# Performance work log

Hardware: AMD Instinct MI355X
Metric: run time of the kernel (lower is better)

Reference implementation:

```python
import jax, jax.numpy as jnp
import numpy as np

L, D = 32768, 1024  # timesteps, independent book-feature columns


def setup_inputs() -> dict:
    key = jax.random.key(0)
    k1, k2 = jax.random.split(key)
    data = jax.random.normal(k1, (L, D), dtype=jnp.float32)
    first_offset = jax.random.normal(k2, (1, D), dtype=jnp.float32)
    alpha = jnp.float32(0.01)  # EWMA smoothing constant in (0, 1)
    return {"data": data, "first_offset": first_offset, "alpha": alpha}


def reference(data, first_offset, alpha):
    # Exact math of ewma_vectorized_safe (vmapped over columns):
    #   y_t = (1 - alpha) * y_{t-1} + alpha * x_t,  y_{-1} = first_offset
    # The original implements this with a chunked power-scaled cumsum trick
    # for precision; a single linear scan computes the identical recurrence.
    decay = 1.0 - alpha

    def step(carry, x_t):  # carry: (D,), x_t: (D,)
        y_t = decay * carry + alpha * x_t
        return y_t, y_t

    last, out = jax.lax.scan(step, first_offset[0], data)  # out: (L, D)
    return out, last[None, :]  # matches (out, out[-1:]) with out_axes=(1, 1)
```

## Files before the change

### kernel.cpp

```cpp
#include <hip/hip_runtime.h>


#define LT   32768
#define DC   1024
#define TCH  32
#define CCH  (LT / TCH)
#define TPB  256
#define D4   (DC / 4)

typedef float nf4 __attribute__((ext_vector_type(4)));

__global__ void ewma_phase1(const nf4* __restrict__ data4,
                            nf4* __restrict__ zend4,
                            const float* __restrict__ alpha_p) {
    const float alpha = alpha_p[0];
    const float decay = 1.0f - alpha;
    const int tid = threadIdx.x;
    const int c = blockIdx.x;
    const nf4* p = data4 + (size_t)c * TCH * D4 + tid;
    float z0 = 0.f, z1 = 0.f, z2 = 0.f, z3 = 0.f;
#pragma unroll 8
    for (int i = 0; i < TCH; ++i) {
        nf4 x = p[(size_t)i * D4];
        z0 = fmaf(decay, z0, alpha * x.x);
        z1 = fmaf(decay, z1, alpha * x.y);
        z2 = fmaf(decay, z2, alpha * x.z);
        z3 = fmaf(decay, z3, alpha * x.w);
    }
    nf4 zv; zv.x = z0; zv.y = z1; zv.z = z2; zv.w = z3;
    zend4[c * D4 + tid] = zv;
}

__global__ void ewma_phase2(const float* __restrict__ zend,
                            const float* __restrict__ first,
                            float* __restrict__ carry,
                            const float* __restrict__ alpha_p) {
    const float alpha = alpha_p[0];
    const float decay = 1.0f - alpha;
    float r = decay;
    r *= r; r *= r; r *= r; r *= r; r *= r;

    const int lane = threadIdx.x & 63;
    const int d = (blockIdx.x * blockDim.x + threadIdx.x) >> 6;
    constexpr int CPL = CCH / 64;

    float e[CPL];
#pragma unroll
    for (int j = 0; j < CPL; ++j)
        e[j] = zend[(lane * CPL + j) * DC + d];

    float A = 0.f;
#pragma unroll
    for (int j = 0; j < CPL; ++j) A = fmaf(r, A, e[j]);

    float q = r;
    q *= q; q *= q; q *= q; q *= q;

    float y = A;
    float p = q;
#pragma unroll
    for (int o = 1; o < 64; o <<= 1) {
        float prev = __shfl_up(y, o, 64);
        if (lane >= o) y = fmaf(p, prev, y);
        p = p * p;
    }
    float excl = __shfl_up(y, 1, 64);
    if (lane == 0) excl = 0.f;

    float qpow = 1.f;
    {
        float base = q;
        int e2 = lane;
        while (e2) { if (e2 & 1) qpow *= base; base *= base; e2 >>= 1; }
    }
    float S = fmaf(qpow, first[d], excl);

#pragma unroll
    for (int j = 0; j < CPL; ++j) {
        const int c = lane * CPL + j;
        carry[c * DC + d] = S;
        S = fmaf(r, S, e[j]);
    }
}

__global__ void ewma_phase3(const nf4* __restrict__ data4,
                            const nf4* __restrict__ carry4,
                            nf4* __restrict__ out4,
                            nf4* __restrict__ out_last4,
                            const float* __restrict__ alpha_p) {
    const float alpha = alpha_p[0];
    const float decay = 1.0f - alpha;
    const int tid = threadIdx.x;
    const int c = blockIdx.x;
    const nf4 cin = carry4[c * D4 + tid];
    const nf4* p = data4 + (size_t)c * TCH * D4 + tid;
    nf4* o = out4 + (size_t)c * TCH * D4 + tid;
    float z0 = 0.f, z1 = 0.f, z2 = 0.f, z3 = 0.f, pw = 1.f;
#pragma unroll 8
    for (int i = 0; i < TCH; ++i) {
        nf4 x = p[(size_t)i * D4];
        z0 = fmaf(decay, z0, alpha * x.x);
        z1 = fmaf(decay, z1, alpha * x.y);
        z2 = fmaf(decay, z2, alpha * x.z);
        z3 = fmaf(decay, z3, alpha * x.w);
        pw *= decay;
        nf4 yv;
        yv.x = fmaf(pw, cin.x, z0);
        yv.y = fmaf(pw, cin.y, z1);
        yv.z = fmaf(pw, cin.z, z2);
        yv.w = fmaf(pw, cin.w, z3);
        __builtin_nontemporal_store(yv, &o[(size_t)i * D4]);
    }
    if (c == CCH - 1) {
        nf4 yl;
        yl.x = fmaf(pw, cin.x, z0);
        yl.y = fmaf(pw, cin.y, z1);
        yl.z = fmaf(pw, cin.z, z2);
        yl.w = fmaf(pw, cin.w, z3);
        out_last4[tid] = yl;
    }
}

extern "C" void kernel_launch(void* const* d_in, const int* in_sizes, int n_in,
                              void* d_out, int out_size, void* d_ws, size_t ws_size,
                              hipStream_t stream) {
    const float* data    = (const float*)d_in[0];
    const float* first   = (const float*)d_in[1];
    const float* alpha_p = (const float*)d_in[2];
    float* out = (float*)d_out;

    float* zend  = (float*)d_ws;
    float* carry = zend + (size_t)CCH * DC;

    ewma_phase1<<<CCH, TPB, 0, stream>>>(
        (const nf4*)data, (nf4*)zend, alpha_p);

    ewma_phase2<<<DC / (TPB / 64), TPB, 0, stream>>>(
        zend, first, carry, alpha_p);

    ewma_phase3<<<CCH, TPB, 0, stream>>>(
        (const nf4*)data, (const nf4*)carry, (nf4*)out,
        (nf4*)(out + (size_t)LT * DC), alpha_p);
}
```

Baseline: 84.50 us.

## Write local scan to output in phase 1 and fix up in place in phase 3

Phase 1 now writes the chunk-local partial scan straight to the output buffer. Phase 3 then reads that buffer back, adds the decayed carry, and writes the result in place instead of re-reading the input and recomputing the scan. Input loads in phase 1 become nontemporal, and phase 3's stores become ordinary cached stores. The aim is better cache behaviour, since the output written in phase 1 may still be resident in the large last-level cache when phase 3 runs. The cost is an extra full-size write pass, so total traffic becomes read+write, then read+write, instead of read, then read+write.

```diff
diff --git a/kernel.cpp b/kernel.cpp
--- a/kernel.cpp
+++ b/kernel.cpp
@@ -10,31 +10,35 @@
 
 typedef float nf4 __attribute__((ext_vector_type(4)));
 
-__global__ void ewma_phase1(const nf4* __restrict__ data4,
-                            nf4* __restrict__ zend4,
-                            const float* __restrict__ alpha_p) {
+__global__ void ewma_k1(const nf4* __restrict__ data4,
+                        nf4* __restrict__ out4,
+                        nf4* __restrict__ zend4,
+                        const float* __restrict__ alpha_p) {
     const float alpha = alpha_p[0];
     const float decay = 1.0f - alpha;
     const int tid = threadIdx.x;
     const int c = blockIdx.x;
     const nf4* p = data4 + (size_t)c * TCH * D4 + tid;
+    nf4* o = out4 + (size_t)c * TCH * D4 + tid;
     float z0 = 0.f, z1 = 0.f, z2 = 0.f, z3 = 0.f;
 #pragma unroll 8
     for (int i = 0; i < TCH; ++i) {
-        nf4 x = p[(size_t)i * D4];
+        nf4 x = __builtin_nontemporal_load(&p[(size_t)i * D4]);
         z0 = fmaf(decay, z0, alpha * x.x);
         z1 = fmaf(decay, z1, alpha * x.y);
         z2 = fmaf(decay, z2, alpha * x.z);
         z3 = fmaf(decay, z3, alpha * x.w);
+        nf4 zv; zv.x = z0; zv.y = z1; zv.z = z2; zv.w = z3;
+        o[(size_t)i * D4] = zv;
     }
-    nf4 zv; zv.x = z0; zv.y = z1; zv.z = z2; zv.w = z3;
-    zend4[c * D4 + tid] = zv;
+    nf4 ze; ze.x = z0; ze.y = z1; ze.z = z2; ze.w = z3;
+    zend4[c * D4 + tid] = ze;
 }
 
-__global__ void ewma_phase2(const float* __restrict__ zend,
-                            const float* __restrict__ first,
-                            float* __restrict__ carry,
-                            const float* __restrict__ alpha_p) {
+__global__ void ewma_k2(const float* __restrict__ zend,
+                        const float* __restrict__ first,
+                        float* __restrict__ carry,
+                        const float* __restrict__ alpha_p) {
     const float alpha = alpha_p[0];
     const float decay = 1.0f - alpha;
     float r = decay;
@@ -83,42 +87,30 @@
     }
 }
 
-__global__ void ewma_phase3(const nf4* __restrict__ data4,
-                            const nf4* __restrict__ carry4,
-                            nf4* __restrict__ out4,
-                            nf4* __restrict__ out_last4,
-                            const float* __restrict__ alpha_p) {
+__global__ void ewma_k3(nf4* __restrict__ out4,
+                        const nf4* __restrict__ carry4,
+                        nf4* __restrict__ out_last4,
+                        const float* __restrict__ alpha_p) {
     const float alpha = alpha_p[0];
     const float decay = 1.0f - alpha;
     const int tid = threadIdx.x;
     const int c = blockIdx.x;
     const nf4 cin = carry4[c * D4 + tid];
-    const nf4* p = data4 + (size_t)c * TCH * D4 + tid;
     nf4* o = out4 + (size_t)c * TCH * D4 + tid;
-    float z0 = 0.f, z1 = 0.f, z2 = 0.f, z3 = 0.f, pw = 1.f;
+    float pw = 1.f;
+    nf4 yv;
 #pragma unroll 8
     for (int i = 0; i < TCH; ++i) {
-        nf4 x = p[(size_t)i * D4];
-        z0 = fmaf(decay, z0, alpha * x.x);
-        z1 = fmaf(decay, z1, alpha * x.y);
-        z2 = fmaf(decay, z2, alpha * x.z);
-        z3 = fmaf(decay, z3, alpha * x.w);
+        nf4 v = o[(size_t)i * D4];
         pw *= decay;
-        nf4 yv;
-        yv.x = fmaf(pw, cin.x, z0);
-        yv.y = fmaf(pw, cin.y, z1);
-        yv.z = fmaf(pw, cin.z, z2);
-        yv.w = fmaf(pw, cin.w, z3);
-        __builtin_nontemporal_store(yv, &o[(size_t)i * D4]);
+        yv.x = fmaf(pw, cin.x, v.x);
+        yv.y = fmaf(pw, cin.y, v.y);
+        yv.z = fmaf(pw, cin.z, v.z);
+        yv.w = fmaf(pw, cin.w, v.w);
+        o[(size_t)i * D4] = yv;
     }
-    if (c == CCH - 1) {
-        nf4 yl;
-        yl.x = fmaf(pw, cin.x, z0);
-        yl.y = fmaf(pw, cin.y, z1);
-        yl.z = fmaf(pw, cin.z, z2);
-        yl.w = fmaf(pw, cin.w, z3);
-        out_last4[tid] = yl;
-    }
+    if (c == CCH - 1)
+        out_last4[tid] = yv;
 }
 
 extern "C" void kernel_launch(void* const* d_in, const int* in_sizes, int n_in,
@@ -132,13 +124,13 @@
     float* zend  = (float*)d_ws;
     float* carry = zend + (size_t)CCH * DC;
 
-    ewma_phase1<<<CCH, TPB, 0, stream>>>(
-        (const nf4*)data, (nf4*)zend, alpha_p);
+    ewma_k1<<<CCH, TPB, 0, stream>>>(
+        (const nf4*)data, (nf4*)out, (nf4*)zend, alpha_p);
 
-    ewma_phase2<<<DC / (TPB / 64), TPB, 0, stream>>>(
+    ewma_k2<<<DC / (TPB / 64), TPB, 0, stream>>>(
         zend, first, carry, alpha_p);
 
-    ewma_phase3<<<CCH, TPB, 0, stream>>>(
-        (const nf4*)data, (const nf4*)carry, (nf4*)out,
+    ewma_k3<<<CCH, TPB, 0, stream>>>(
+        (nf4*)out, (const nf4*)carry,
         (nf4*)(out + (size_t)LT * DC), alpha_p);
 }
```

Result: slower. 106.7 us (+26.2%).

## Split columns into two slabs so phase-3 data reads hit cache

Applied to the files above, without the earlier changes.

Runs the three-phase scan as two sequential passes over column halves, each pass launching phase 1, 2 and 3 on a 64 MB data slab with 128-thread blocks. The intent is for phase 3 to re-read data still resident in the large last-level cache after phase 1, rather than fetching it again from HBM. Loops are also fully unrolled, and output stores become regular stores instead of nontemporal ones. The cost is twice as many kernel launches, smaller blocks, and normal stores that may evict cached input.

```diff
diff --git a/kernel.cpp b/kernel.cpp
--- a/kernel.cpp
+++ b/kernel.cpp
@@ -3,23 +3,25 @@
 
 #define LT   32768
 #define DC   1024
+#define NS   2
+#define SW   (DC / NS)
+#define SW4  (SW / 4)
 #define TCH  32
 #define CCH  (LT / TCH)
-#define TPB  256
 #define D4   (DC / 4)
 
 typedef float nf4 __attribute__((ext_vector_type(4)));
 
-__global__ void ewma_phase1(const nf4* __restrict__ data4,
-                            nf4* __restrict__ zend4,
-                            const float* __restrict__ alpha_p) {
+__global__ void ewma_p1(const nf4* __restrict__ data4,
+                        nf4* __restrict__ zend4,
+                        const float* __restrict__ alpha_p, int s) {
     const float alpha = alpha_p[0];
     const float decay = 1.0f - alpha;
-    const int tid = threadIdx.x;
+    const int g = threadIdx.x;
     const int c = blockIdx.x;
-    const nf4* p = data4 + (size_t)c * TCH * D4 + tid;
+    const nf4* p = data4 + (size_t)c * TCH * D4 + s * SW4 + g;
     float z0 = 0.f, z1 = 0.f, z2 = 0.f, z3 = 0.f;
-#pragma unroll 8
+#pragma unroll
     for (int i = 0; i < TCH; ++i) {
         nf4 x = p[(size_t)i * D4];
         z0 = fmaf(decay, z0, alpha * x.x);
@@ -28,26 +30,26 @@
         z3 = fmaf(decay, z3, alpha * x.w);
     }
     nf4 zv; zv.x = z0; zv.y = z1; zv.z = z2; zv.w = z3;
-    zend4[c * D4 + tid] = zv;
+    zend4[(size_t)c * D4 + s * SW4 + g] = zv;
 }
 
-__global__ void ewma_phase2(const float* __restrict__ zend,
-                            const float* __restrict__ first,
-                            float* __restrict__ carry,
-                            const float* __restrict__ alpha_p) {
+__global__ void ewma_p2(const float* __restrict__ zend,
+                        const float* __restrict__ first,
+                        float* __restrict__ carry,
+                        const float* __restrict__ alpha_p, int s) {
     const float alpha = alpha_p[0];
     const float decay = 1.0f - alpha;
     float r = decay;
     r *= r; r *= r; r *= r; r *= r; r *= r;
 
     const int lane = threadIdx.x & 63;
-    const int d = (blockIdx.x * blockDim.x + threadIdx.x) >> 6;
+    const int d = s * SW + ((blockIdx.x * blockDim.x + threadIdx.x) >> 6);
     constexpr int CPL = CCH / 64;
 
     float e[CPL];
 #pragma unroll
     for (int j = 0; j < CPL; ++j)
-        e[j] = zend[(lane * CPL + j) * DC + d];
+        e[j] = zend[(size_t)(lane * CPL + j) * DC + d];
 
     float A = 0.f;
 #pragma unroll
@@ -78,25 +80,25 @@
 #pragma unroll
     for (int j = 0; j < CPL; ++j) {
         const int c = lane * CPL + j;
-        carry[c * DC + d] = S;
+        carry[(size_t)c * DC + d] = S;
         S = fmaf(r, S, e[j]);
     }
 }
 
-__global__ void ewma_phase3(const nf4* __restrict__ data4,
-                            const nf4* __restrict__ carry4,
-                            nf4* __restrict__ out4,
-                            nf4* __restrict__ out_last4,
-                            const float* __restrict__ alpha_p) {
+__global__ void ewma_p3(const nf4* __restrict__ data4,
+                        const nf4* __restrict__ carry4,
+                        nf4* __restrict__ out4,
+                        nf4* __restrict__ out_last4,
+                        const float* __restrict__ alpha_p, int s) {
     const float alpha = alpha_p[0];
     const float decay = 1.0f - alpha;
-    const int tid = threadIdx.x;
+    const int g = threadIdx.x;
     const int c = blockIdx.x;
-    const nf4 cin = carry4[c * D4 + tid];
-    const nf4* p = data4 + (size_t)c * TCH * D4 + tid;
-    nf4* o = out4 + (size_t)c * TCH * D4 + tid;
+    const nf4 cin = carry4[(size_t)c * D4 + s * SW4 + g];
+    const nf4* p = data4 + (size_t)c * TCH * D4 + s * SW4 + g;
+    nf4* o = out4 + (size_t)c * TCH * D4 + s * SW4 + g;
     float z0 = 0.f, z1 = 0.f, z2 = 0.f, z3 = 0.f, pw = 1.f;
-#pragma unroll 8
+#pragma unroll
     for (int i = 0; i < TCH; ++i) {
         nf4 x = p[(size_t)i * D4];
         z0 = fmaf(decay, z0, alpha * x.x);
@@ -109,7 +111,7 @@
         yv.y = fmaf(pw, cin.y, z1);
         yv.z = fmaf(pw, cin.z, z2);
         yv.w = fmaf(pw, cin.w, z3);
-        __builtin_nontemporal_store(yv, &o[(size_t)i * D4]);
+        o[(size_t)i * D4] = yv;
     }
     if (c == CCH - 1) {
         nf4 yl;
@@ -117,7 +119,7 @@
         yl.y = fmaf(pw, cin.y, z1);
         yl.z = fmaf(pw, cin.z, z2);
         yl.w = fmaf(pw, cin.w, z3);
-        out_last4[tid] = yl;
+        out_last4[s * SW4 + g] = yl;
     }
 }
 
@@ -132,13 +134,15 @@
     float* zend  = (float*)d_ws;
     float* carry = zend + (size_t)CCH * DC;
 
-    ewma_phase1<<<CCH, TPB, 0, stream>>>(
-        (const nf4*)data, (nf4*)zend, alpha_p);
+    for (int s = 0; s < NS; ++s) {
+        ewma_p1<<<CCH, SW4, 0, stream>>>(
+            (const nf4*)data, (nf4*)zend, alpha_p, s);
 
-    ewma_phase2<<<DC / (TPB / 64), TPB, 0, stream>>>(
-        zend, first, carry, alpha_p);
+        ewma_p2<<<SW / 4, 256, 0, stream>>>(
+            zend, first, carry, alpha_p, s);
 
-    ewma_phase3<<<CCH, TPB, 0, stream>>>(
-        (const nf4*)data, (const nf4*)carry, (nf4*)out,
-        (nf4*)(out + (size_t)LT * DC), alpha_p);
+        ewma_p3<<<CCH, SW4, 0, stream>>>(
+            (const nf4*)data, (const nf4*)carry, (nf4*)out,
+            (nf4*)(out + (size_t)LT * DC), alpha_p, s);
+    }
 }
```

Result: slower. 100.2 us (+18.6%).

## Fuse three EWMA phases into one cooperative kernel with grid syncs

Applied to the files above, without the earlier changes.

Merges the chunk-reduce, carry-scan, and apply phases into a single cooperative launch separated by grid-wide barriers, and doubles the time chunk length so the whole grid fits co-resident. This removes the inter-kernel launch gaps and halves the intermediate carry buffers. It trades occupancy and grid-sync cost for this, and also replaces nontemporal output stores with regular stores.

```diff
diff --git a/kernel.cpp b/kernel.cpp
--- a/kernel.cpp
+++ b/kernel.cpp
@@ -1,123 +1,126 @@
 #include <hip/hip_runtime.h>
+#include <hip/hip_cooperative_groups.h>
+
+namespace cg = cooperative_groups;
 
 
 #define LT   32768
 #define DC   1024
-#define TCH  32
+#define TCH  64
 #define CCH  (LT / TCH)
 #define TPB  256
 #define D4   (DC / 4)
 
 typedef float nf4 __attribute__((ext_vector_type(4)));
 
-__global__ void ewma_phase1(const nf4* __restrict__ data4,
-                            nf4* __restrict__ zend4,
-                            const float* __restrict__ alpha_p) {
+__global__ __launch_bounds__(TPB, 2)
+void ewma_fused(const nf4* __restrict__ data4,
+                const float* __restrict__ first,
+                const float* __restrict__ alpha_p,
+                nf4* __restrict__ out4,
+                nf4* __restrict__ zend4,
+                float* __restrict__ carry) {
+    cg::grid_group grid = cg::this_grid();
     const float alpha = alpha_p[0];
     const float decay = 1.0f - alpha;
     const int tid = threadIdx.x;
     const int c = blockIdx.x;
-    const nf4* p = data4 + (size_t)c * TCH * D4 + tid;
-    float z0 = 0.f, z1 = 0.f, z2 = 0.f, z3 = 0.f;
+
+    {
+        const nf4* p = data4 + (size_t)c * TCH * D4 + tid;
+        float z0 = 0.f, z1 = 0.f, z2 = 0.f, z3 = 0.f;
 #pragma unroll 8
-    for (int i = 0; i < TCH; ++i) {
-        nf4 x = p[(size_t)i * D4];
-        z0 = fmaf(decay, z0, alpha * x.x);
-        z1 = fmaf(decay, z1, alpha * x.y);
-        z2 = fmaf(decay, z2, alpha * x.z);
-        z3 = fmaf(decay, z3, alpha * x.w);
+        for (int i = 0; i < TCH; ++i) {
+            nf4 x = p[(size_t)i * D4];
+            z0 = fmaf(decay, z0, alpha * x.x);
+            z1 = fmaf(decay, z1, alpha * x.y);
+            z2 = fmaf(decay, z2, alpha * x.z);
+            z3 = fmaf(decay, z3, alpha * x.w);
+        }
+        nf4 zv; zv.x = z0; zv.y = z1; zv.z = z2; zv.w = z3;
+        zend4[(size_t)c * D4 + tid] = zv;
     }
-    nf4 zv; zv.x = z0; zv.y = z1; zv.z = z2; zv.w = z3;
-    zend4[c * D4 + tid] = zv;
-}
 
-__global__ void ewma_phase2(const float* __restrict__ zend,
-                            const float* __restrict__ first,
-                            float* __restrict__ carry,
-                            const float* __restrict__ alpha_p) {
-    const float alpha = alpha_p[0];
-    const float decay = 1.0f - alpha;
-    float r = decay;
-    r *= r; r *= r; r *= r; r *= r; r *= r;
+    grid.sync();
 
-    const int lane = threadIdx.x & 63;
-    const int d = (blockIdx.x * blockDim.x + threadIdx.x) >> 6;
-    constexpr int CPL = CCH / 64;
+    if (c < DC / 4) {
+        const int lane = tid & 63;
+        const int w = tid >> 6;
+        const int d = c * 4 + w;
+        float r = decay;
+        r *= r; r *= r; r *= r; r *= r; r *= r; r *= r;
+        constexpr int CPL = CCH / 64;
 
-    float e[CPL];
+        const float* zend = (const float*)zend4;
+        float e[CPL];
 #pragma unroll
-    for (int j = 0; j < CPL; ++j)
-        e[j] = zend[(lane * CPL + j) * DC + d];
+        for (int j = 0; j < CPL; ++j)
+            e[j] = zend[(size_t)(lane * CPL + j) * DC + d];
 
-    float A = 0.f;
+        float A = 0.f;
 #pragma unroll
-    for (int j = 0; j < CPL; ++j) A = fmaf(r, A, e[j]);
+        for (int j = 0; j < CPL; ++j) A = fmaf(r, A, e[j]);
 
-    float q = r;
-    q *= q; q *= q; q *= q; q *= q;
+        float q = r;
+        q *= q; q *= q; q *= q;
 
-    float y = A;
-    float p = q;
+        float y = A;
+        float pq = q;
 #pragma unroll
-    for (int o = 1; o < 64; o <<= 1) {
-        float prev = __shfl_up(y, o, 64);
-        if (lane >= o) y = fmaf(p, prev, y);
-        p = p * p;
-    }
-    float excl = __shfl_up(y, 1, 64);
-    if (lane == 0) excl = 0.f;
+        for (int o = 1; o < 64; o <<= 1) {
+            float prev = __shfl_up(y, o, 64);
+            if (lane >= o) y = fmaf(pq, prev, y);
+            pq = pq * pq;
+        }
+        float excl = __shfl_up(y, 1, 64);
+        if (lane == 0) excl = 0.f;
 
-    float qpow = 1.f;
-    {
-        float base = q;
-        int e2 = lane;
-        while (e2) { if (e2 & 1) qpow *= base; base *= base; e2 >>= 1; }
-    }
-    float S = fmaf(qpow, first[d], excl);
+        float qpow = 1.f;
+        {
+            float base = q;
+            int e2 = lane;
+            while (e2) { if (e2 & 1) qpow *= base; base *= base; e2 >>= 1; }
+        }
+        float S = fmaf(qpow, first[d], excl);
 
 #pragma unroll
-    for (int j = 0; j < CPL; ++j) {
-        const int c = lane * CPL + j;
-        carry[c * DC + d] = S;
-        S = fmaf(r, S, e[j]);
+        for (int j = 0; j < CPL; ++j) {
+            const int cc = lane * CPL + j;
+            carry[(size_t)cc * DC + d] = S;
+            S = fmaf(r, S, e[j]);
+        }
     }
-}
 
-__global__ void ewma_phase3(const nf4* __restrict__ data4,
-                            const nf4* __restrict__ carry4,
-                            nf4* __restrict__ out4,
-                            nf4* __restrict__ out_last4,
-                            const float* __restrict__ alpha_p) {
-    const float alpha = alpha_p[0];
-    const float decay = 1.0f - alpha;
-    const int tid = threadIdx.x;
-    const int c = blockIdx.x;
-    const nf4 cin = carry4[c * D4 + tid];
-    const nf4* p = data4 + (size_t)c * TCH * D4 + tid;
-    nf4* o = out4 + (size_t)c * TCH * D4 + tid;
-    float z0 = 0.f, z1 = 0.f, z2 = 0.f, z3 = 0.f, pw = 1.f;
+    grid.sync();
+
+    {
+        const nf4 cin = ((const nf4*)carry)[(size_t)c * D4 + tid];
+        const nf4* p = data4 + (size_t)c * TCH * D4 + tid;
+        nf4* o = out4 + (size_t)c * TCH * D4 + tid;
+        float z0 = 0.f, z1 = 0.f, z2 = 0.f, z3 = 0.f, pw = 1.f;
 #pragma unroll 8
-    for (int i = 0; i < TCH; ++i) {
-        nf4 x = p[(size_t)i * D4];
-        z0 = fmaf(decay, z0, alpha * x.x);
-        z1 = fmaf(decay, z1, alpha * x.y);
-        z2 = fmaf(decay, z2, alpha * x.z);
-        z3 = fmaf(decay, z3, alpha * x.w);
-        pw *= decay;
-        nf4 yv;
-        yv.x = fmaf(pw, cin.x, z0);
-        yv.y = fmaf(pw, cin.y, z1);
-        yv.z = fmaf(pw, cin.z, z2);
-        yv.w = fmaf(pw, cin.w, z3);
-        __builtin_nontemporal_store(yv, &o[(size_t)i * D4]);
-    }
-    if (c == CCH - 1) {
-        nf4 yl;
-        yl.x = fmaf(pw, cin.x, z0);
-        yl.y = fmaf(pw, cin.y, z1);
-        yl.z = fmaf(pw, cin.z, z2);
-        yl.w = fmaf(pw, cin.w, z3);
-        out_last4[tid] = yl;
+        for (int i = 0; i < TCH; ++i) {
+            nf4 x = p[(size_t)i * D4];
+            z0 = fmaf(decay, z0, alpha * x.x);
+            z1 = fmaf(decay, z1, alpha * x.y);
+            z2 = fmaf(decay, z2, alpha * x.z);
+            z3 = fmaf(decay, z3, alpha * x.w);
+            pw *= decay;
+            nf4 yv;
+            yv.x = fmaf(pw, cin.x, z0);
+            yv.y = fmaf(pw, cin.y, z1);
+            yv.z = fmaf(pw, cin.z, z2);
+            yv.w = fmaf(pw, cin.w, z3);
+            o[(size_t)i * D4] = yv;
+        }
+        if (c == CCH - 1) {
+            nf4 yl;
+            yl.x = fmaf(pw, cin.x, z0);
+            yl.y = fmaf(pw, cin.y, z1);
+            yl.z = fmaf(pw, cin.z, z2);
+            yl.w = fmaf(pw, cin.w, z3);
+            ((nf4*)(((float*)out4) + (size_t)LT * DC))[tid] = yl;
+        }
     }
 }
 
@@ -132,13 +135,12 @@
     float* zend  = (float*)d_ws;
     float* carry = zend + (size_t)CCH * DC;
 
-    ewma_phase1<<<CCH, TPB, 0, stream>>>(
-        (const nf4*)data, (nf4*)zend, alpha_p);
+    const nf4* data4 = (const nf4*)data;
+    nf4* out4 = (nf4*)out;
+    nf4* zend4 = (nf4*)zend;
 
-    ewma_phase2<<<DC / (TPB / 64), TPB, 0, stream>>>(
-        zend, first, carry, alpha_p);
-
-    ewma_phase3<<<CCH, TPB, 0, stream>>>(
-        (const nf4*)data, (const nf4*)carry, (nf4*)out,
-        (nf4*)(out + (size_t)LT * DC), alpha_p);
+    void* args[] = { (void*)&data4, (void*)&first, (void*)&alpha_p,
+                     (void*)&out4, (void*)&zend4, (void*)&carry };
+    hipLaunchCooperativeKernel((const void*)ewma_fused,
+                               dim3(CCH), dim3(TPB), args, 0, stream);
 }
```

New measurement: 201.8 us. 139% more time.
